# Kernel tuning notes

Measured on AMD Instinct MI355X. Metric: run time of the kernel, lower is better.

## Reference

```python
import jax, jax.numpy as jnp
import numpy as np

B, N, DX, DR, H, DOUT = 4, 384, 2, 128, 128, 64


def setup_inputs() -> dict:
    key = jax.random.key(0)
    ks = jax.random.split(key, 6)
    return {
        "r": jax.random.normal(ks[0], (B, DR), dtype=jnp.float32),
        "x_ctx": jax.random.normal(ks[1], (B, N, DX), dtype=jnp.float32),
        "y_ctx": jax.random.normal(ks[2], (B, N, 1), dtype=jnp.float32),
        "x_trg": jax.random.normal(ks[3], (B, 256, DX), dtype=jnp.float32),
        "W1": jax.random.normal(ks[4], (DX + DR, H), dtype=jnp.float32) * (1.0 / np.sqrt(DX + DR)),
        "b1": jnp.zeros((H,), dtype=jnp.float32),
        "W2": jax.random.normal(ks[5], (H, DOUT), dtype=jnp.float32) * (1.0 / np.sqrt(H)),
        "b2": jnp.zeros((DOUT,), dtype=jnp.float32),
    }


def reference(r, x_ctx, y_ctx, x_trg, W1, b1, W2, b2):
    # Pairwise differences over the context set: [B, N, N, DX]
    x_diff = x_ctx[:, :, None, :] - x_ctx[:, None, :, :]
    # Broadcast the context representation over the pair grid: [B, N, N, DR]
    n = x_ctx.shape[1]
    r_rep = jnp.broadcast_to(r[:, None, None, :], (r.shape[0], n, n, r.shape[-1]))
    # Concat then pointwise deepset MLP (Linear -> ReLU -> Linear)
    z = jnp.concatenate([x_diff, r_rep], axis=-1)  # [B, N, N, DX+DR]
    h = jax.nn.relu(jnp.einsum('bnmd,dh->bnmh', z, W1) + b1)
    out = jnp.einsum('bnmh,ho->bnmo', h, W2) + b2  # [B, N, N, DOUT]
    return out
```

## Files before the change

### kernel.cpp

```cpp
#include <hip/hip_runtime.h>


typedef __attribute__((ext_vector_type(8))) __bf16 bf16x8;
typedef __attribute__((ext_vector_type(4))) float f32x4;

#define B_    4
#define N_    384
#define H_    128
#define DOUT_ 64

__global__ __launch_bounds__(256, 2) void te_fused(
    const float* __restrict__ r, const float* __restrict__ xctx,
    const float* __restrict__ W1, const float* __restrict__ b1,
    const float* __restrict__ W2, const float* __restrict__ b2,
    float* __restrict__ out)
{
    __shared__ __align__(16) float xs[N_ * 2];
    __shared__ __align__(16) float cpart[2][H_];
    __shared__ __align__(16) float tbuf[4][16][64];

    const int tid  = threadIdx.x;
    const int wave = tid >> 6, lane = tid & 63;
    const int g = lane >> 4, rl = lane & 15;

    const int bid = blockIdx.x;
    const int b = bid / N_, n = bid - b * N_;

    {
        const int k = tid & 127, dh = tid >> 7;
        float acc = dh ? 0.f : b1[k];
        const float* wc = W1 + (2 + dh * 64) * H_ + k;
        const float* rb = r + b * 128 + dh * 64;
        #pragma unroll 8
        for (int d = 0; d < 64; ++d) acc = fmaf(rb[d], wc[d * H_], acc);
        cpart[dh][k] = acc;
    }
    if (tid < 192)
        *reinterpret_cast<f32x4*>(&xs[tid * 4]) =
            *reinterpret_cast<const f32x4*>(xctx + b * (N_ * 2) + tid * 4);

    bf16x8 w2f[4][4];
    #pragma unroll
    for (int rt = 0; rt < 4; ++rt) {
        const float* wp = W2 + rt * 16 + rl;
        #pragma unroll
        for (int ks = 0; ks < 4; ++ks)
            #pragma unroll
            for (int jj = 0; jj < 8; ++jj) {
                const int kk = ks * 32 + ((jj >> 2) << 4) + (g << 2) + (jj & 3);
                w2f[rt][ks][jj] = (__bf16)wp[kk * DOUT_];
            }
    }

    f32x4 w1a[4][2], w1b[4][2], cf[4][2], b2f[4];
    #pragma unroll
    for (int ks = 0; ks < 4; ++ks)
        #pragma unroll
        for (int hh = 0; hh < 2; ++hh) {
            const int kk = ks * 32 + hh * 16 + (g << 2);
            w1a[ks][hh] = *reinterpret_cast<const f32x4*>(W1 + kk);
            w1b[ks][hh] = *reinterpret_cast<const f32x4*>(W1 + H_ + kk);
        }
    #pragma unroll
    for (int rt = 0; rt < 4; ++rt)
        b2f[rt] = *reinterpret_cast<const f32x4*>(b2 + rt * 16 + (g << 2));

    __syncthreads();

    #pragma unroll
    for (int ks = 0; ks < 4; ++ks)
        #pragma unroll
        for (int hh = 0; hh < 2; ++hh) {
            const int kk = ks * 32 + hh * 16 + (g << 2);
            cf[ks][hh] = *reinterpret_cast<const f32x4*>(&cpart[0][kk]) +
                         *reinterpret_cast<const f32x4*>(&cpart[1][kk]);
        }

    const float x0n = xs[2 * n], x1n = xs[2 * n + 1];
    float* tb = &tbuf[wave][0][0];
    const int cb2 = lane & 15;
    float* const outn = out + ((size_t)(b * N_ + n)) * N_ * DOUT_;

    for (int t = 0; t < 6; ++t) {
        const int mbase = wave * 96 + t * 16;
        const int m = mbase + rl;
        const float dx0 = x0n - xs[2 * m];
        const float dx1 = x1n - xs[2 * m + 1];

        bf16x8 hf[4];
        #pragma unroll
        for (int ks = 0; ks < 4; ++ks)
            #pragma unroll
            for (int hh = 0; hh < 2; ++hh)
                #pragma unroll
                for (int j = 0; j < 4; ++j) {
                    float hp = fmaf(dx1, w1b[ks][hh][j],
                               fmaf(dx0, w1a[ks][hh][j], cf[ks][hh][j]));
                    hf[ks][hh * 4 + j] = (__bf16)(hp > 0.f ? hp : 0.f);
                }

        f32x4 acc[4];
        #pragma unroll
        for (int rt = 0; rt < 4; ++rt) acc[rt] = b2f[rt];
        #pragma unroll
        for (int ks = 0; ks < 4; ++ks)
            #pragma unroll
            for (int rt = 0; rt < 4; ++rt)
                acc[rt] = __builtin_amdgcn_mfma_f32_16x16x32_bf16(w2f[rt][ks], hf[ks], acc[rt], 0, 0, 0);

        #pragma unroll
        for (int rt = 0; rt < 4; ++rt) {
            const int cblk = ((rt << 2) | g) ^ rl;
            *reinterpret_cast<f32x4*>(tb + (rl << 6) + (cblk << 2)) = acc[rt];
        }
        float* onp = outn + (size_t)mbase * DOUT_;
        #pragma unroll
        for (int q = 0; q < 4; ++q) {
            const int mm = (lane >> 4) | (q << 2);
            f32x4 rowv = *reinterpret_cast<const f32x4*>(tb + (mm << 6) + ((cb2 ^ mm) << 2));
            *reinterpret_cast<f32x4*>(onp + mm * DOUT_ + (cb2 << 2)) = rowv;
        }
    }
}

extern "C" void kernel_launch(void* const* d_in, const int* in_sizes, int n_in,
                              void* d_out, int out_size, void* d_ws, size_t ws_size,
                              hipStream_t stream)
{
    const float* r    = (const float*)d_in[0];
    const float* xctx = (const float*)d_in[1];
    const float* W1 = (const float*)d_in[4];
    const float* b1 = (const float*)d_in[5];
    const float* W2 = (const float*)d_in[6];
    const float* b2 = (const float*)d_in[7];
    float* out = (float*)d_out;

    hipLaunchKernelGGL(te_fused, dim3(B_ * N_), dim3(256), 0, stream,
                       r, xctx, W1, b1, W2, b2, out);
}
```

Measured before the change: 40.56 us.

## Split output columns across two waves per block with shared h rows

Blocks shrink from four waves to two, and the work is split differently. Each wave now owns 32 of the 64 output columns over all 384 m rows, where before each wave owned every column for its own 96 rows. Each wave holds only half of W2 in registers, and the two waves meet through a double-buffered LDS transpose guarded by a __syncthreads each iteration, so they can write full 256-byte output rows together. This lowers register pressure and W2 load work, and the launch bounds now target three blocks per CU. The cost is that every wave recomputes the full first-layer h tile, doubling VALU work per output, and a block-wide barrier now sits in the loop.

```diff
diff --git a/kernel.cpp b/kernel.cpp
--- a/kernel.cpp
+++ b/kernel.cpp
@@ -3,56 +3,61 @@
 
 typedef __attribute__((ext_vector_type(8))) __bf16 bf16x8;
 typedef __attribute__((ext_vector_type(4))) float f32x4;
+typedef __attribute__((ext_vector_type(2))) float f32x2;
 
 #define B_    4
 #define N_    384
 #define H_    128
 #define DOUT_ 64
 
-__global__ __launch_bounds__(256, 2) void te_fused(
+__global__ __launch_bounds__(128, 3) void te_fused(
     const float* __restrict__ r, const float* __restrict__ xctx,
     const float* __restrict__ W1, const float* __restrict__ b1,
     const float* __restrict__ W2, const float* __restrict__ b2,
     float* __restrict__ out)
 {
     __shared__ __align__(16) float xs[N_ * 2];
-    __shared__ __align__(16) float cpart[2][H_];
-    __shared__ __align__(16) float tbuf[4][16][64];
+    __shared__ __align__(16) float cs[H_];
+    __shared__ __align__(16) float tbuf[2][2][16][64];
 
     const int tid  = threadIdx.x;
-    const int wave = tid >> 6, lane = tid & 63;
-    const int g = lane >> 4, rl = lane & 15;
+    const int w    = tid >> 6, lane = tid & 63;
+    const int g    = lane >> 4, rl = lane & 15;
 
     const int bid = blockIdx.x;
     const int b = bid / N_, n = bid - b * N_;
 
     {
-        const int k = tid & 127, dh = tid >> 7;
-        float acc = dh ? 0.f : b1[k];
-        const float* wc = W1 + (2 + dh * 64) * H_ + k;
-        const float* rb = r + b * 128 + dh * 64;
+        float acc = b1[tid];
+        const float* wc = W1 + 2 * H_ + tid;
+        const float* rb = r + b * 128;
         #pragma unroll 8
-        for (int d = 0; d < 64; ++d) acc = fmaf(rb[d], wc[d * H_], acc);
-        cpart[dh][k] = acc;
+        for (int d = 0; d < 128; ++d) acc = fmaf(rb[d], wc[d * H_], acc);
+        cs[tid] = acc;
     }
-    if (tid < 192)
+    {
+        const float* xb = xctx + b * (N_ * 2);
         *reinterpret_cast<f32x4*>(&xs[tid * 4]) =
-            *reinterpret_cast<const f32x4*>(xctx + b * (N_ * 2) + tid * 4);
+            *reinterpret_cast<const f32x4*>(xb + tid * 4);
+        if (tid < 64)
+            *reinterpret_cast<f32x4*>(&xs[(128 + tid) * 4]) =
+                *reinterpret_cast<const f32x4*>(xb + (128 + tid) * 4);
+    }
 
-    bf16x8 w2f[4][4];
+    bf16x8 w2f[2][4];
     #pragma unroll
-    for (int rt = 0; rt < 4; ++rt) {
-        const float* wp = W2 + rt * 16 + rl;
+    for (int ot = 0; ot < 2; ++ot) {
+        const float* wp = W2 + w * 32 + ot * 16 + rl;
         #pragma unroll
         for (int ks = 0; ks < 4; ++ks)
             #pragma unroll
             for (int jj = 0; jj < 8; ++jj) {
                 const int kk = ks * 32 + ((jj >> 2) << 4) + (g << 2) + (jj & 3);
-                w2f[rt][ks][jj] = (__bf16)wp[kk * DOUT_];
+                w2f[ot][ks][jj] = (__bf16)wp[kk * DOUT_];
             }
     }
 
-    f32x4 w1a[4][2], w1b[4][2], cf[4][2], b2f[4];
+    f32x4 w1a[4][2], w1b[4][2], cf[4][2], b2f[2];
     #pragma unroll
     for (int ks = 0; ks < 4; ++ks)
         #pragma unroll
@@ -62,63 +67,67 @@
             w1b[ks][hh] = *reinterpret_cast<const f32x4*>(W1 + H_ + kk);
         }
     #pragma unroll
-    for (int rt = 0; rt < 4; ++rt)
-        b2f[rt] = *reinterpret_cast<const f32x4*>(b2 + rt * 16 + (g << 2));
+    for (int ot = 0; ot < 2; ++ot)
+        b2f[ot] = *reinterpret_cast<const f32x4*>(b2 + w * 32 + ot * 16 + (g << 2));
 
     __syncthreads();
 
     #pragma unroll
     for (int ks = 0; ks < 4; ++ks)
         #pragma unroll
-        for (int hh = 0; hh < 2; ++hh) {
-            const int kk = ks * 32 + hh * 16 + (g << 2);
-            cf[ks][hh] = *reinterpret_cast<const f32x4*>(&cpart[0][kk]) +
-                         *reinterpret_cast<const f32x4*>(&cpart[1][kk]);
+        for (int hh = 0; hh < 2; ++hh)
+            cf[ks][hh] = *reinterpret_cast<const f32x4*>(&cs[ks * 32 + hh * 16 + (g << 2)]);
+
+    const float x0n = xs[2 * n], x1n = xs[2 * n + 1];
+    float* const outn = out + ((size_t)(b * N_ + n)) * N_ * DOUT_;
+    const int ob2 = tid & 15;
+    const int mr0 = tid >> 4;
+
+    for (int tp = 0; tp < 12; ++tp) {
+        const int s = tp & 1;
+
+        #pragma unroll
+        for (int half = 0; half < 2; ++half) {
+            const int m = tp * 32 + half * 16 + rl;
+            const f32x2 xp = *reinterpret_cast<const f32x2*>(&xs[2 * m]);
+            const float dx0 = x0n - xp[0], dx1 = x1n - xp[1];
+
+            bf16x8 hf[4];
+            #pragma unroll
+            for (int ks = 0; ks < 4; ++ks)
+                #pragma unroll
+                for (int hh = 0; hh < 2; ++hh)
+                    #pragma unroll
+                    for (int j = 0; j < 4; ++j) {
+                        float hp = fmaf(dx1, w1b[ks][hh][j],
+                                   fmaf(dx0, w1a[ks][hh][j], cf[ks][hh][j]));
+                        hf[ks][hh * 4 + j] = (__bf16)(hp > 0.f ? hp : 0.f);
+                    }
+
+            f32x4 acc0 = b2f[0], acc1 = b2f[1];
+            #pragma unroll
+            for (int ks = 0; ks < 4; ++ks) {
+                acc0 = __builtin_amdgcn_mfma_f32_16x16x32_bf16(w2f[0][ks], hf[ks], acc0, 0, 0, 0);
+                acc1 = __builtin_amdgcn_mfma_f32_16x16x32_bf16(w2f[1][ks], hf[ks], acc1, 0, 0, 0);
+            }
+
+            {
+                const int ob0 = (w << 3) | g;
+                *reinterpret_cast<f32x4*>(&tbuf[s][half][rl][(ob0 ^ rl) << 2]) = acc0;
+                const int ob1 = (w << 3) | 4 | g;
+                *reinterpret_cast<f32x4*>(&tbuf[s][half][rl][(ob1 ^ rl) << 2]) = acc1;
+            }
         }
 
-    const float x0n = xs[2 * n], x1n = xs[2 * n + 1];
-    float* tb = &tbuf[wave][0][0];
-    const int cb2 = lane & 15;
-    float* const outn = out + ((size_t)(b * N_ + n)) * N_ * DOUT_;
+        __syncthreads();
 
-    for (int t = 0; t < 6; ++t) {
-        const int mbase = wave * 96 + t * 16;
-        const int m = mbase + rl;
-        const float dx0 = x0n - xs[2 * m];
-        const float dx1 = x1n - xs[2 * m + 1];
-
-        bf16x8 hf[4];
+        float* const onp = outn + (size_t)(tp * 32) * DOUT_;
         #pragma unroll
-        for (int ks = 0; ks < 4; ++ks)
-            #pragma unroll
-            for (int hh = 0; hh < 2; ++hh)
-                #pragma unroll
-                for (int j = 0; j < 4; ++j) {
-                    float hp = fmaf(dx1, w1b[ks][hh][j],
-                               fmaf(dx0, w1a[ks][hh][j], cf[ks][hh][j]));
-                    hf[ks][hh * 4 + j] = (__bf16)(hp > 0.f ? hp : 0.f);
-                }
-
-        f32x4 acc[4];
-        #pragma unroll
-        for (int rt = 0; rt < 4; ++rt) acc[rt] = b2f[rt];
-        #pragma unroll
-        for (int ks = 0; ks < 4; ++ks)
-            #pragma unroll
-            for (int rt = 0; rt < 4; ++rt)
-                acc[rt] = __builtin_amdgcn_mfma_f32_16x16x32_bf16(w2f[rt][ks], hf[ks], acc[rt], 0, 0, 0);
-
-        #pragma unroll
-        for (int rt = 0; rt < 4; ++rt) {
-            const int cblk = ((rt << 2) | g) ^ rl;
-            *reinterpret_cast<f32x4*>(tb + (rl << 6) + (cblk << 2)) = acc[rt];
-        }
-        float* onp = outn + (size_t)mbase * DOUT_;
-        #pragma unroll
-        for (int q = 0; q < 4; ++q) {
-            const int mm = (lane >> 4) | (q << 2);
-            f32x4 rowv = *reinterpret_cast<const f32x4*>(tb + (mm << 6) + ((cb2 ^ mm) << 2));
-            *reinterpret_cast<f32x4*>(onp + mm * DOUT_ + (cb2 << 2)) = rowv;
+        for (int p = 0; p < 4; ++p) {
+            const int sub = p >> 1;
+            const int mr  = mr0 + ((p & 1) << 3);
+            f32x4 rv = *reinterpret_cast<const f32x4*>(&tbuf[s][sub][mr][(ob2 ^ mr) << 2]);
+            *reinterpret_cast<f32x4*>(onp + (size_t)(sub * 16 + mr) * DOUT_ + (ob2 << 2)) = rv;
         }
     }
 }
@@ -135,6 +144,6 @@
     const float* b2 = (const float*)d_in[7];
     float* out = (float*)d_out;
 
-    hipLaunchKernelGGL(te_fused, dim3(B_ * N_), dim3(256), 0, stream,
+    hipLaunchKernelGGL(te_fused, dim3(B_ * N_), dim3(128), 0, stream,
                        r, xctx, W1, b1, W2, b2, out);
 }
```

After: 40.71 us. Within noise of the previous version (+0.4%).
